# Optimization experiments

Measured on AMD Instinct MI355X. Metric: run time of the kernel, lower is better.

The kernel has to match this reference:

```python
import jax, jax.numpy as jnp
import numpy as np

N = 20000      # nodes
G = 400        # distinct TCR group ids
D_IN, H1, H2, D_OUT = 128, 256, 256, 128
LN_EPS = 1e-5


def _init_linear(key, fan_in, fan_out):
    s = 1.0 / np.sqrt(fan_in)
    return jax.random.uniform(key, (fan_in, fan_out), jnp.float32, -s, s)


def setup_inputs() -> dict:
    key = jax.random.key(0)
    ks = jax.random.split(key, 6)
    x = jax.random.normal(ks[0], (N, D_IN), jnp.float32)
    idx_TCR = jax.random.randint(ks[1], (N,), 0, G, dtype=jnp.int64)
    W1 = _init_linear(ks[2], D_IN, H1)
    W2 = _init_linear(ks[3], H1, H2)
    W3 = _init_linear(ks[4], H2, D_OUT)
    b1 = jnp.zeros((H1,), jnp.float32)
    b2 = jnp.zeros((H2,), jnp.float32)
    b3 = jnp.zeros((D_OUT,), jnp.float32)
    gamma = jnp.ones((D_OUT,), jnp.float32)
    beta = jnp.zeros((D_OUT,), jnp.float32)
    return {"x": x, "idx_TCR": idx_TCR, "W1": W1, "b1": b1,
            "W2": W2, "b2": b2, "W3": W3, "b3": b3,
            "gamma": gamma, "beta": beta}


def _build_edges(idx_TCR):
    # construct_graph: connect node pairs with equal idx, upper triangle only
    # (directed src<tgt edges, as in the torch code), then append self-loops
    # as PyG GCNConv.gcn_norm does.
    idx = np.asarray(idx_TCR).reshape(-1)
    n = idx.shape[0]
    eq = idx[:, None] == idx[None, :]
    src, tgt = np.nonzero(np.triu(eq, k=1))
    loop = np.arange(n)
    row = jnp.asarray(np.concatenate([src, loop]))  # message source
    col = jnp.asarray(np.concatenate([tgt, loop]))  # message target
    return row, col, n


def _gcn_norm(row, col, n, dtype):
    # degree from incoming edges (incl. self-loops), symmetric normalization
    deg = jax.ops.segment_sum(jnp.ones(row.shape[0], dtype), col, num_segments=n)
    dis = jnp.where(deg > 0, jax.lax.rsqrt(deg), jnp.zeros_like(deg))
    return dis[row] * dis[col]  # [E]


def _gcn_conv(x, W, b, row, col, norm, n):
    h = x @ W                                   # [N, out]
    msg = h[row] * norm[:, None]                # gather + scale, [E, out]
    out = jax.ops.segment_sum(msg, col, num_segments=n)  # scatter-add
    return out + b


def reference(x, idx_TCR, W1, b1, W2, b2, W3, b3, gamma, beta):
    row, col, n = _build_edges(idx_TCR)
    norm = _gcn_norm(row, col, n, x.dtype)
    h = jax.nn.relu(_gcn_conv(x, W1, b1, row, col, norm, n))
    h = jax.nn.relu(_gcn_conv(h, W2, b2, row, col, norm, n))
    h = jax.nn.relu(_gcn_conv(h, W3, b3, row, col, norm, n))
    # LayerNorm over last dim
    mu = h.mean(axis=-1, keepdims=True)
    var = ((h - mu) ** 2).mean(axis=-1, keepdims=True)
    return (h - mu) * jax.lax.rsqrt(var + LN_EPS) * gamma + beta
```

## Files before the change

### kernel.cpp

```cpp
#include <hip/hip_runtime.h>
#include <hip/hip_bf16.h>

#define NN 20000
#define NG 400
#define D_IN 128
#define H1 256
#define H2 256
#define D_OUT 128
#define WT_ELEMS (D_IN * H1 + H1 * H2 + H2 * D_OUT)
#define MCAP 1024
#define WSLOT 256

#define STY 72
#define ST1 136
#define ST2 264
#define ST3 264
#define SF  132
#define REGB 36864

typedef __attribute__((ext_vector_type(8))) short short8;
typedef __attribute__((ext_vector_type(4))) short short4v;
typedef __attribute__((ext_vector_type(4))) float floatx4;

__device__ __forceinline__ short f2b(float f) {
    __hip_bfloat16 h = __float2bfloat16(f);
    return *(short*)&h;
}


__global__ __launch_bounds__(256) void wt_all(
    const float* __restrict__ W1, const float* __restrict__ W2,
    const float* __restrict__ W3, __hip_bfloat16* __restrict__ Wt1,
    __hip_bfloat16* __restrict__ Wt2, __hip_bfloat16* __restrict__ Wt3)
{
    int o = blockIdx.x * 256 + threadIdx.x;
    if (o < D_IN * H1) {
        int n = o / D_IN, k = o - n * D_IN;
        Wt1[o] = __float2bfloat16(W1[(size_t)k * H1 + n]);
    } else if (o < D_IN * H1 + H1 * H2) {
        int p = o - D_IN * H1;
        int n = p / H1, k = p - n * H1;
        Wt2[p] = __float2bfloat16(W2[(size_t)k * H2 + n]);
    } else if (o < WT_ELEMS) {
        int p = o - D_IN * H1 - H1 * H2;
        int n = p / H2, k = p - n * H2;
        Wt3[p] = __float2bfloat16(W3[(size_t)k * D_OUT + n]);
    }
}


__global__ __launch_bounds__(512) void fused_gcn(
    const float* __restrict__ x, const int* __restrict__ idx,
    const __hip_bfloat16* __restrict__ Wt1_,
    const __hip_bfloat16* __restrict__ Wt2_,
    const __hip_bfloat16* __restrict__ Wt3_,
    const float* __restrict__ b1, const float* __restrict__ b2,
    const float* __restrict__ b3,
    const float* __restrict__ gamma, const float* __restrict__ beta,
    float* __restrict__ out)
{
    __shared__ __align__(16) char RA[REGB];
    __shared__ __align__(16) char RB[REGB];
    __shared__ int mlist[MCAP];
    __shared__ int wcnt[8];

    int tid = threadIdx.x;
    int w = tid >> 6;
    int lane = tid & 63;
    int quad = lane >> 4;
    int l15 = lane & 15;
    int g = blockIdx.x;

    int* WS = (int*)RA;
    {
        int slice = w * 625;
        int wcount = 0;
        unsigned long long lowm = (1ull << lane) - 1ull;
#pragma unroll
        for (int b2i = 0; b2i < 2; ++b2i) {
            int4 v[5];
#pragma unroll
            for (int r = 0; r < 5; ++r) {
                int q = (b2i * 5 + r) * 64 + lane;
                v[r] = (q < 625) ? *(const int4*)&idx[(slice + q) * 4]
                                 : make_int4(-1, -1, -1, -1);
            }
#pragma unroll
            for (int r = 0; r < 5; ++r) {
                bool f0 = (v[r].x == g), f1 = (v[r].y == g);
                bool f2 = (v[r].z == g), f3 = (v[r].w == g);
                unsigned long long m0 = __ballot(f0), m1 = __ballot(f1);
                unsigned long long m2 = __ballot(f2), m3 = __ballot(f3);
                int p = wcount + __popcll(m0 & lowm) + __popcll(m1 & lowm)
                               + __popcll(m2 & lowm) + __popcll(m3 & lowm);
                int j0 = (slice + (b2i * 5 + r) * 64 + lane) * 4;
                int e0 = (int)f0, e1 = (int)f1, e2 = (int)f2;
                if (f0 && p < WSLOT)                WS[w * WSLOT + p] = j0;
                if (f1 && p + e0 < WSLOT)           WS[w * WSLOT + p + e0] = j0 + 1;
                if (f2 && p + e0 + e1 < WSLOT)      WS[w * WSLOT + p + e0 + e1] = j0 + 2;
                if (f3 && p + e0 + e1 + e2 < WSLOT) WS[w * WSLOT + p + e0 + e1 + e2] = j0 + 3;
                wcount += __popcll(m0) + __popcll(m1) + __popcll(m2) + __popcll(m3);
            }
        }
        if (lane == 0) wcnt[w] = min(wcount, WSLOT);
    }
    __syncthreads();
    int cnt = 0;
    {
        int myprefix = 0;
#pragma unroll
        for (int ww = 0; ww < 8; ++ww) {
            int c = wcnt[ww];
            if (ww < w) myprefix += c;
            cnt += c;
        }
        cnt = min(cnt, MCAP);
        int myc = wcnt[w];
        for (int k = lane; k < myc; k += 64) {
            int dstp = myprefix + k;
            if (dstp < MCAP) mlist[dstp] = WS[w * WSLOT + k];
        }
    }
    if (cnt <= 0) return;

    float2 gmv = *(const float2*)&gamma[lane * 2];
    float2 btv = *(const float2*)&beta[lane * 2];
    float4 bb1[2], bb2[2], bb3;
#pragma unroll
    for (int i = 0; i < 2; ++i) {
        bb1[i] = *(const float4*)&b1[(2 * w + i) * 16 + quad * 4];
        bb2[i] = *(const float4*)&b2[(2 * w + i) * 16 + quad * 4];
    }
    bb3 = *(const float4*)&b3[w * 16 + quad * 4];

    __syncthreads();

    auto ltfrag = [&](int nt, int k2) -> short8 {
        int thr = nt * 16 + l15 - k2 * 32 - quad * 8;
        short8 f;
#pragma unroll
        for (int e = 0; e < 8; ++e)
            f[e] = (e <= thr) ? (short)0x3F80 : (short)0;
        return f;
    };

    float c1[2][4], c2[2][4], c3[4];
#pragma unroll
    for (int r = 0; r < 4; ++r) {
        c1[0][r] = 0.f; c1[1][r] = 0.f;
        c2[0][r] = 0.f; c2[1][r] = 0.f;
        c3[r] = 0.f;
    }

    const short* wt1p = (const short*)Wt1_;
    const short* wt2p = (const short*)Wt2_;
    const short* wt3p = (const short*)Wt3_;

    for (int base = 0; base < cnt; base += 64) {
        asm("" : "+s"(wt1p), "+s"(wt2p), "+s"(wt3p));
        int mt = min(64, cnt - base);
        int par = (base >> 6) & 1;
        char* Rc = par ? RB : RA;
        char* Rd = par ? RA : RB;
        short* T1 = (short*)Rc;
        short* T2 = (short*)Rc;
        short* T3 = (short*)Rc;
        float* F  = (float*)Rc;
        short* Yt = (short*)Rd;

        float djn[4];
#pragma unroll
        for (int nt = 0; nt < 4; ++nt)
            djn[nt] = rsqrtf((float)(base + nt * 16 + l15 + 1));

        {
            int row = (lane >> 3) + 8 * w;
            int mr = base + row;
            int nid = mlist[mr < cnt ? mr : cnt - 1];
            float sdr = rsqrtf((float)(mr + 1));
            const float* xp = x + (size_t)nid * D_IN + (lane & 7) * 4;
#pragma unroll
            for (int t = 0; t < 4; ++t) {
                float4 v = *(const float4*)(xp + t * 32);
                short4v o;
                o[0] = f2b(v.x * sdr); o[1] = f2b(v.y * sdr);
                o[2] = f2b(v.z * sdr); o[3] = f2b(v.w * sdr);
                *(short4v*)&T1[row * ST1 + (lane & 7) * 4 + t * 32] = o;
            }
        }
        __syncthreads();

        {
            floatx4 acc[4][2];
#pragma unroll
            for (int i = 0; i < 4; ++i) { acc[i][0] = (floatx4)0.0f; acc[i][1] = (floatx4)0.0f; }
#pragma unroll
            for (int kk = 0; kk < 4; ++kk) {
                short8 a4[4], bw[2];
#pragma unroll
                for (int i = 0; i < 4; ++i)
                    a4[i] = *(const short8*)&T1[(i * 16 + l15) * ST1 + kk * 32 + quad * 8];
#pragma unroll
                for (int nt = 0; nt < 2; ++nt)
                    bw[nt] = *(const short8*)&wt1p[((size_t)((w * 2 + nt) * 16 + l15)) * D_IN + kk * 32 + quad * 8];
#pragma unroll
                for (int i = 0; i < 4; ++i)
#pragma unroll
                    for (int nt = 0; nt < 2; ++nt)
                        acc[i][nt] = __builtin_amdgcn_mfma_f32_16x16x32_bf16(
                            a4[i], bw[nt], acc[i][nt], 0, 0, 0);
            }
#pragma unroll
            for (int i = 0; i < 4; ++i)
#pragma unroll
                for (int nt = 0; nt < 2; ++nt) {
                    short4v o4;
#pragma unroll
                    for (int r = 0; r < 4; ++r) o4[r] = f2b(acc[i][nt][r]);
                    *(short4v*)&Yt[((w * 2 + nt) * 16 + l15) * STY + i * 16 + quad * 4] = o4;
                }
        }
        __syncthreads();

        {
            floatx4 acc[2][4];
#pragma unroll
            for (int i = 0; i < 2; ++i)
#pragma unroll
                for (int nt = 0; nt < 4; ++nt) acc[i][nt] = (floatx4)0.0f;
#pragma unroll
            for (int k2 = 0; k2 < 2; ++k2) {
                short8 af[2];
#pragma unroll
                for (int i = 0; i < 2; ++i)
                    af[i] = *(const short8*)&Yt[((2 * w + i) * 16 + l15) * STY + k2 * 32 + quad * 8];
#pragma unroll
                for (int nt = 0; nt < 4; ++nt) {
                    short8 lt = ltfrag(nt, k2);
#pragma unroll
                    for (int i = 0; i < 2; ++i)
                        acc[i][nt] = __builtin_amdgcn_mfma_f32_16x16x32_bf16(
                            af[i], lt, acc[i][nt], 0, 0, 0);
                }
            }
#pragma unroll
            for (int i = 0; i < 2; ++i) {
                float nc[4] = {0.f, 0.f, 0.f, 0.f};
#pragma unroll
                for (int nt = 0; nt < 4; ++nt) {
                    float tmp[4];
#pragma unroll
                    for (int r = 0; r < 4; ++r) tmp[r] = acc[i][nt][r] + c1[i][r];
                    if (nt == 3) {
#pragma unroll
                        for (int r = 0; r < 4; ++r) nc[r] = tmp[r];
                    }
                    short4v o4;
                    o4[0] = f2b(fmaxf(tmp[0] * djn[nt] + bb1[i].x, 0.0f) * djn[nt]);
                    o4[1] = f2b(fmaxf(tmp[1] * djn[nt] + bb1[i].y, 0.0f) * djn[nt]);
                    o4[2] = f2b(fmaxf(tmp[2] * djn[nt] + bb1[i].z, 0.0f) * djn[nt]);
                    o4[3] = f2b(fmaxf(tmp[3] * djn[nt] + bb1[i].w, 0.0f) * djn[nt]);
                    *(short4v*)&T2[(nt * 16 + l15) * ST2 + (2 * w + i) * 16 + quad * 4] = o4;
                }
#pragma unroll
                for (int r = 0; r < 4; ++r)
                    c1[i][r] = __shfl(nc[r], (lane & 48) + 15);
            }
        }
        __syncthreads();

        {
            floatx4 acc[4][2];
#pragma unroll
            for (int i = 0; i < 4; ++i) { acc[i][0] = (floatx4)0.0f; acc[i][1] = (floatx4)0.0f; }
#pragma unroll
            for (int kk = 0; kk < 8; ++kk) {
                short8 a4[4], bw[2];
#pragma unroll
                for (int i = 0; i < 4; ++i)
                    a4[i] = *(const short8*)&T2[(i * 16 + l15) * ST2 + kk * 32 + quad * 8];
#pragma unroll
                for (int nt = 0; nt < 2; ++nt)
                    bw[nt] = *(const short8*)&wt2p[((size_t)((w * 2 + nt) * 16 + l15)) * H1 + kk * 32 + quad * 8];
#pragma unroll
                for (int i = 0; i < 4; ++i)
#pragma unroll
                    for (int nt = 0; nt < 2; ++nt)
                        acc[i][nt] = __builtin_amdgcn_mfma_f32_16x16x32_bf16(
                            a4[i], bw[nt], acc[i][nt], 0, 0, 0);
            }
#pragma unroll
            for (int i = 0; i < 4; ++i)
#pragma unroll
                for (int nt = 0; nt < 2; ++nt) {
                    short4v o4;
#pragma unroll
                    for (int r = 0; r < 4; ++r) o4[r] = f2b(acc[i][nt][r]);
                    *(short4v*)&Yt[((w * 2 + nt) * 16 + l15) * STY + i * 16 + quad * 4] = o4;
                }
        }
        __syncthreads();

        {
            floatx4 acc[2][4];
#pragma unroll
            for (int i = 0; i < 2; ++i)
#pragma unroll
                for (int nt = 0; nt < 4; ++nt) acc[i][nt] = (floatx4)0.0f;
#pragma unroll
            for (int k2 = 0; k2 < 2; ++k2) {
                short8 af[2];
#pragma unroll
                for (int i = 0; i < 2; ++i)
                    af[i] = *(const short8*)&Yt[((2 * w + i) * 16 + l15) * STY + k2 * 32 + quad * 8];
#pragma unroll
                for (int nt = 0; nt < 4; ++nt) {
                    short8 lt = ltfrag(nt, k2);
#pragma unroll
                    for (int i = 0; i < 2; ++i)
                        acc[i][nt] = __builtin_amdgcn_mfma_f32_16x16x32_bf16(
                            af[i], lt, acc[i][nt], 0, 0, 0);
                }
            }
#pragma unroll
            for (int i = 0; i < 2; ++i) {
                float nc[4] = {0.f, 0.f, 0.f, 0.f};
#pragma unroll
                for (int nt = 0; nt < 4; ++nt) {
                    float tmp[4];
#pragma unroll
                    for (int r = 0; r < 4; ++r) tmp[r] = acc[i][nt][r] + c2[i][r];
                    if (nt == 3) {
#pragma unroll
                        for (int r = 0; r < 4; ++r) nc[r] = tmp[r];
                    }
                    short4v o4;
                    o4[0] = f2b(fmaxf(tmp[0] * djn[nt] + bb2[i].x, 0.0f) * djn[nt]);
                    o4[1] = f2b(fmaxf(tmp[1] * djn[nt] + bb2[i].y, 0.0f) * djn[nt]);
                    o4[2] = f2b(fmaxf(tmp[2] * djn[nt] + bb2[i].z, 0.0f) * djn[nt]);
                    o4[3] = f2b(fmaxf(tmp[3] * djn[nt] + bb2[i].w, 0.0f) * djn[nt]);
                    *(short4v*)&T3[(nt * 16 + l15) * ST3 + (2 * w + i) * 16 + quad * 4] = o4;
                }
#pragma unroll
                for (int r = 0; r < 4; ++r)
                    c2[i][r] = __shfl(nc[r], (lane & 48) + 15);
            }
        }
        __syncthreads();

        {
            floatx4 acc[4];
#pragma unroll
            for (int i = 0; i < 4; ++i) acc[i] = (floatx4)0.0f;
#pragma unroll
            for (int kk = 0; kk < 8; ++kk) {
                short8 bw = *(const short8*)&wt3p[((size_t)(w * 16 + l15)) * H2 + kk * 32 + quad * 8];
#pragma unroll
                for (int i = 0; i < 4; ++i) {
                    short8 a4 = *(const short8*)&T3[(i * 16 + l15) * ST3 + kk * 32 + quad * 8];
                    acc[i] = __builtin_amdgcn_mfma_f32_16x16x32_bf16(a4, bw, acc[i], 0, 0, 0);
                }
            }
#pragma unroll
            for (int i = 0; i < 4; ++i) {
                short4v o4;
#pragma unroll
                for (int r = 0; r < 4; ++r) o4[r] = f2b(acc[i][r]);
                *(short4v*)&Yt[(w * 16 + l15) * STY + i * 16 + quad * 4] = o4;
            }
        }
        __syncthreads();

        {
            floatx4 acc[4];
#pragma unroll
            for (int nt = 0; nt < 4; ++nt) acc[nt] = (floatx4)0.0f;
#pragma unroll
            for (int k2 = 0; k2 < 2; ++k2) {
                short8 af = *(const short8*)&Yt[(w * 16 + l15) * STY + k2 * 32 + quad * 8];
#pragma unroll
                for (int nt = 0; nt < 4; ++nt)
                    acc[nt] = __builtin_amdgcn_mfma_f32_16x16x32_bf16(
                        af, ltfrag(nt, k2), acc[nt], 0, 0, 0);
            }
            float nc[4] = {0.f, 0.f, 0.f, 0.f};
#pragma unroll
            for (int nt = 0; nt < 4; ++nt) {
                float tmp[4];
#pragma unroll
                for (int r = 0; r < 4; ++r) tmp[r] = acc[nt][r] + c3[r];
                if (nt == 3) {
#pragma unroll
                    for (int r = 0; r < 4; ++r) nc[r] = tmp[r];
                }
                float4 o;
                o.x = fmaxf(tmp[0] * djn[nt] + bb3.x, 0.0f);
                o.y = fmaxf(tmp[1] * djn[nt] + bb3.y, 0.0f);
                o.z = fmaxf(tmp[2] * djn[nt] + bb3.z, 0.0f);
                o.w = fmaxf(tmp[3] * djn[nt] + bb3.w, 0.0f);
                *(float4*)&F[(nt * 16 + l15) * SF + w * 16 + quad * 4] = o;
            }
#pragma unroll
            for (int r = 0; r < 4; ++r)
                c3[r] = __shfl(nc[r], (lane & 48) + 15);
        }
        __syncthreads();

        for (int r = w; r < mt; r += 8) {
            float2 v = *(const float2*)&F[r * SF + lane * 2];
            float s1 = v.x + v.y;
            float s2v = v.x * v.x + v.y * v.y;
#pragma unroll
            for (int off = 32; off > 0; off >>= 1) {
                s1 += __shfl_down(s1, off);
                s2v += __shfl_down(s2v, off);
            }
            s1 = __shfl(s1, 0);
            s2v = __shfl(s2v, 0);
            float mu = s1 * (1.0f / D_OUT);
            float var = s2v * (1.0f / D_OUT) - mu * mu;
            float rstd = rsqrtf(var + 1e-5f);
            float2 o;
            o.x = (v.x - mu) * rstd * gmv.x + btv.x;
            o.y = (v.y - mu) * rstd * gmv.y + btv.y;
            *(float2*)&out[(size_t)mlist[base + r] * D_OUT + lane * 2] = o;
        }
    }
}


extern "C" void kernel_launch(void* const* d_in, const int* in_sizes, int n_in,
                              void* d_out, int out_size, void* d_ws, size_t ws_size,
                              hipStream_t stream) {
    const float* x     = (const float*)d_in[0];
    const int*   idx   = (const int*)d_in[1];
    const float* W1    = (const float*)d_in[2];
    const float* b1    = (const float*)d_in[3];
    const float* W2    = (const float*)d_in[4];
    const float* b2    = (const float*)d_in[5];
    const float* W3    = (const float*)d_in[6];
    const float* b3    = (const float*)d_in[7];
    const float* gamma = (const float*)d_in[8];
    const float* beta  = (const float*)d_in[9];
    float* out = (float*)d_out;

    char* ws = (char*)d_ws;
    size_t off = 0;
    auto alloc = [&](size_t bytes) -> void* {
        void* p = (void*)(ws + off);
        off += (bytes + 255) & ~(size_t)255;
        return p;
    };
    __hip_bfloat16* Wt1 = (__hip_bfloat16*)alloc((size_t)D_IN * H1 * 2);
    __hip_bfloat16* Wt2 = (__hip_bfloat16*)alloc((size_t)H1 * H2 * 2);
    __hip_bfloat16* Wt3 = (__hip_bfloat16*)alloc((size_t)H2 * D_OUT * 2);

    wt_all<<<(WT_ELEMS + 255) / 256, 256, 0, stream>>>(
        W1, W2, W3, Wt1, Wt2, Wt3);

    fused_gcn<<<NG, 512, 0, stream>>>(
        x, idx, Wt1, Wt2, Wt3, b1, b2, b3, gamma, beta, out);
}
```

Baseline: 127.5 us.

## Process two groups per block with four waves each

Each block now handles two TCR groups, with the 8 waves split into two teams of 4, each team doing twice the column work per stage. The grid is halved to 200 blocks, which fits a single wave of blocks on the CUs and halves the per-block idx scan cost per group. LDS doubles to about 147KB, so occupancy stays at one block per CU. Each team does twice the serial MFMA work, and the loop runs to the larger of the two group counts, so the block waits on its slower group.

```diff
diff --git a/kernel.cpp b/kernel.cpp
--- a/kernel.cpp
+++ b/kernel.cpp
@@ -8,7 +8,7 @@
 #define H2 256
 #define D_OUT 128
 #define WT_ELEMS (D_IN * H1 + H1 * H2 + H2 * D_OUT)
-#define MCAP 1024
+#define MC2 512
 #define WSLOT 256
 
 #define STY 72
@@ -16,7 +16,7 @@
 #define ST2 264
 #define ST3 264
 #define SF  132
-#define REGB 36864
+#define PIPEB 73728
 
 typedef __attribute__((ext_vector_type(8))) short short8;
 typedef __attribute__((ext_vector_type(4))) short short4v;
@@ -59,22 +59,25 @@
     const float* __restrict__ gamma, const float* __restrict__ beta,
     float* __restrict__ out)
 {
-    __shared__ __align__(16) char RA[REGB];
-    __shared__ __align__(16) char RB[REGB];
-    __shared__ int mlist[MCAP];
-    __shared__ int wcnt[8];
+    __shared__ __align__(16) char LB[2 * PIPEB];
+    __shared__ int mlist0[MC2], mlist1[MC2];
+    __shared__ int wcnt0[8], wcnt1[8];
 
     int tid = threadIdx.x;
     int w = tid >> 6;
     int lane = tid & 63;
     int quad = lane >> 4;
     int l15 = lane & 15;
-    int g = blockIdx.x;
-
-    int* WS = (int*)RA;
+    int p = w >> 2;
+    int u = w & 3;
+    int g0 = blockIdx.x * 2;
+    int g1 = g0 + 1;
+
+    int* WS0 = (int*)LB;
+    int* WS1 = (int*)(LB + 8192);
     {
         int slice = w * 625;
-        int wcount = 0;
+        int wc0 = 0, wc1 = 0;
         unsigned long long lowm = (1ull << lane) - 1ull;
 #pragma unroll
         for (int b2i = 0; b2i < 2; ++b2i) {
@@ -87,53 +90,71 @@
             }
 #pragma unroll
             for (int r = 0; r < 5; ++r) {
-                bool f0 = (v[r].x == g), f1 = (v[r].y == g);
-                bool f2 = (v[r].z == g), f3 = (v[r].w == g);
-                unsigned long long m0 = __ballot(f0), m1 = __ballot(f1);
-                unsigned long long m2 = __ballot(f2), m3 = __ballot(f3);
-                int p = wcount + __popcll(m0 & lowm) + __popcll(m1 & lowm)
-                               + __popcll(m2 & lowm) + __popcll(m3 & lowm);
                 int j0 = (slice + (b2i * 5 + r) * 64 + lane) * 4;
-                int e0 = (int)f0, e1 = (int)f1, e2 = (int)f2;
-                if (f0 && p < WSLOT)                WS[w * WSLOT + p] = j0;
-                if (f1 && p + e0 < WSLOT)           WS[w * WSLOT + p + e0] = j0 + 1;
-                if (f2 && p + e0 + e1 < WSLOT)      WS[w * WSLOT + p + e0 + e1] = j0 + 2;
-                if (f3 && p + e0 + e1 + e2 < WSLOT) WS[w * WSLOT + p + e0 + e1 + e2] = j0 + 3;
-                wcount += __popcll(m0) + __popcll(m1) + __popcll(m2) + __popcll(m3);
-            }
-        }
-        if (lane == 0) wcnt[w] = min(wcount, WSLOT);
+                {
+                    bool f0 = (v[r].x == g0), f1 = (v[r].y == g0);
+                    bool f2 = (v[r].z == g0), f3 = (v[r].w == g0);
+                    unsigned long long m0 = __ballot(f0), m1 = __ballot(f1);
+                    unsigned long long m2 = __ballot(f2), m3 = __ballot(f3);
+                    int pp = wc0 + __popcll(m0 & lowm) + __popcll(m1 & lowm)
+                                 + __popcll(m2 & lowm) + __popcll(m3 & lowm);
+                    int e0 = (int)f0, e1 = (int)f1, e2 = (int)f2;
+                    if (f0 && pp < WSLOT)                WS0[w * WSLOT + pp] = j0;
+                    if (f1 && pp + e0 < WSLOT)           WS0[w * WSLOT + pp + e0] = j0 + 1;
+                    if (f2 && pp + e0 + e1 < WSLOT)      WS0[w * WSLOT + pp + e0 + e1] = j0 + 2;
+                    if (f3 && pp + e0 + e1 + e2 < WSLOT) WS0[w * WSLOT + pp + e0 + e1 + e2] = j0 + 3;
+                    wc0 += __popcll(m0) + __popcll(m1) + __popcll(m2) + __popcll(m3);
+                }
+                {
+                    bool f0 = (v[r].x == g1), f1 = (v[r].y == g1);
+                    bool f2 = (v[r].z == g1), f3 = (v[r].w == g1);
+                    unsigned long long m0 = __ballot(f0), m1 = __ballot(f1);
+                    unsigned long long m2 = __ballot(f2), m3 = __ballot(f3);
+                    int pp = wc1 + __popcll(m0 & lowm) + __popcll(m1 & lowm)
+                                 + __popcll(m2 & lowm) + __popcll(m3 & lowm);
+                    int e0 = (int)f0, e1 = (int)f1, e2 = (int)f2;
+                    if (f0 && pp < WSLOT)                WS1[w * WSLOT + pp] = j0;
+                    if (f1 && pp + e0 < WSLOT)           WS1[w * WSLOT + pp + e0] = j0 + 1;
+                    if (f2 && pp + e0 + e1 < WSLOT)      WS1[w * WSLOT + pp + e0 + e1] = j0 + 2;
+                    if (f3 && pp + e0 + e1 + e2 < WSLOT) WS1[w * WSLOT + pp + e0 + e1 + e2] = j0 + 3;
+                    wc1 += __popcll(m0) + __popcll(m1) + __popcll(m2) + __popcll(m3);
+                }
+            }
+        }
+        if (lane == 0) { wcnt0[w] = min(wc0, WSLOT); wcnt1[w] = min(wc1, WSLOT); }
     }
     __syncthreads();
-    int cnt = 0;
+    int cnt0 = 0, cnt1 = 0;
     {
-        int myprefix = 0;
+        int pre0 = 0, pre1 = 0;
 #pragma unroll
         for (int ww = 0; ww < 8; ++ww) {
-            int c = wcnt[ww];
-            if (ww < w) myprefix += c;
-            cnt += c;
-        }
-        cnt = min(cnt, MCAP);
-        int myc = wcnt[w];
-        for (int k = lane; k < myc; k += 64) {
-            int dstp = myprefix + k;
-            if (dstp < MCAP) mlist[dstp] = WS[w * WSLOT + k];
+            int c0 = wcnt0[ww], c1w = wcnt1[ww];
+            if (ww < w) { pre0 += c0; pre1 += c1w; }
+            cnt0 += c0; cnt1 += c1w;
+        }
+        cnt0 = min(cnt0, MC2); cnt1 = min(cnt1, MC2);
+        int myc0 = wcnt0[w], myc1 = wcnt1[w];
+        for (int k = lane; k < myc0; k += 64) {
+            int dstp = pre0 + k;
+            if (dstp < MC2) mlist0[dstp] = WS0[w * WSLOT + k];
+        }
+        for (int k = lane; k < myc1; k += 64) {
+            int dstp = pre1 + k;
+            if (dstp < MC2) mlist1[dstp] = WS1[w * WSLOT + k];
         }
     }
-    if (cnt <= 0) return;
+    int cmax = max(cnt0, cnt1);
+    if (cmax <= 0) return;
 
     float2 gmv = *(const float2*)&gamma[lane * 2];
     float2 btv = *(const float2*)&beta[lane * 2];
-    float4 bb1[2], bb2[2], bb3;
-#pragma unroll
-    for (int i = 0; i < 2; ++i) {
-        bb1[i] = *(const float4*)&b1[(2 * w + i) * 16 + quad * 4];
-        bb2[i] = *(const float4*)&b2[(2 * w + i) * 16 + quad * 4];
-    }
-    bb3 = *(const float4*)&b3[w * 16 + quad * 4];
 
     __syncthreads();
+
+    int mycnt = p ? cnt1 : cnt0;
+    int* mylist = p ? mlist1 : mlist0;
+    char* PB = LB + p * PIPEB;
 
     auto ltfrag = [&](int nt, int k2) -> short8 {
         int thr = nt * 16 + l15 - k2 * 32 - quad * 8;
@@ -144,24 +165,26 @@
         return f;
     };
 
-    float c1[2][4], c2[2][4], c3[4];
-#pragma unroll
-    for (int r = 0; r < 4; ++r) {
-        c1[0][r] = 0.f; c1[1][r] = 0.f;
-        c2[0][r] = 0.f; c2[1][r] = 0.f;
-        c3[r] = 0.f;
-    }
+    float c1[2][2][4], c2[2][2][4], c3[2][4];
+#pragma unroll
+    for (int hf = 0; hf < 2; ++hf)
+#pragma unroll
+        for (int r = 0; r < 4; ++r) {
+            c1[hf][0][r] = 0.f; c1[hf][1][r] = 0.f;
+            c2[hf][0][r] = 0.f; c2[hf][1][r] = 0.f;
+            c3[hf][r] = 0.f;
+        }
 
     const short* wt1p = (const short*)Wt1_;
     const short* wt2p = (const short*)Wt2_;
     const short* wt3p = (const short*)Wt3_;
 
-    for (int base = 0; base < cnt; base += 64) {
+    for (int base = 0; base < cmax; base += 64) {
         asm("" : "+s"(wt1p), "+s"(wt2p), "+s"(wt3p));
-        int mt = min(64, cnt - base);
+        int mt = min(64, mycnt - base);
         int par = (base >> 6) & 1;
-        char* Rc = par ? RB : RA;
-        char* Rd = par ? RA : RB;
+        char* Rc = PB + (par ? 36864 : 0);
+        char* Rd = PB + (par ? 0 : 36864);
         short* T1 = (short*)Rc;
         short* T2 = (short*)Rc;
         short* T3 = (short*)Rc;
@@ -173,10 +196,13 @@
         for (int nt = 0; nt < 4; ++nt)
             djn[nt] = rsqrtf((float)(base + nt * 16 + l15 + 1));
 
-        {
-            int row = (lane >> 3) + 8 * w;
+#pragma unroll
+        for (int hf = 0; hf < 2; ++hf) {
+            int hw = hf * 4 + u;
+            int row = (lane >> 3) + 8 * hw;
             int mr = base + row;
-            int nid = mlist[mr < cnt ? mr : cnt - 1];
+            int mi = (mr < mycnt) ? mr : (mycnt > 0 ? mycnt - 1 : 0);
+            int nid = (mycnt > 0) ? mylist[mi] : 0;
             float sdr = rsqrtf((float)(mr + 1));
             const float* xp = x + (size_t)nid * D_IN + (lane & 7) * 4;
 #pragma unroll
@@ -190,7 +216,9 @@
         }
         __syncthreads();
 
-        {
+#pragma unroll
+        for (int hf = 0; hf < 2; ++hf) {
+            int hw = hf * 4 + u;
             floatx4 acc[4][2];
 #pragma unroll
             for (int i = 0; i < 4; ++i) { acc[i][0] = (floatx4)0.0f; acc[i][1] = (floatx4)0.0f; }
@@ -202,7 +230,7 @@
                     a4[i] = *(const short8*)&T1[(i * 16 + l15) * ST1 + kk * 32 + quad * 8];
 #pragma unroll
                 for (int nt = 0; nt < 2; ++nt)
-                    bw[nt] = *(const short8*)&wt1p[((size_t)((w * 2 + nt) * 16 + l15)) * D_IN + kk * 32 + quad * 8];
+                    bw[nt] = *(const short8*)&wt1p[((size_t)((hw * 2 + nt) * 16 + l15)) * D_IN + kk * 32 + quad * 8];
 #pragma unroll
                 for (int i = 0; i < 4; ++i)
 #pragma unroll
@@ -217,12 +245,14 @@
                     short4v o4;
 #pragma unroll
                     for (int r = 0; r < 4; ++r) o4[r] = f2b(acc[i][nt][r]);
-                    *(short4v*)&Yt[((w * 2 + nt) * 16 + l15) * STY + i * 16 + quad * 4] = o4;
-                }
-        }
-        __syncthreads();
-
-        {
+                    *(short4v*)&Yt[((hw * 2 + nt) * 16 + l15) * STY + i * 16 + quad * 4] = o4;
+                }
+        }
+        __syncthreads();
+
+#pragma unroll
+        for (int hf = 0; hf < 2; ++hf) {
+            int hw = hf * 4 + u;
             floatx4 acc[2][4];
 #pragma unroll
             for (int i = 0; i < 2; ++i)
@@ -233,7 +263,7 @@
                 short8 af[2];
 #pragma unroll
                 for (int i = 0; i < 2; ++i)
-                    af[i] = *(const short8*)&Yt[((2 * w + i) * 16 + l15) * STY + k2 * 32 + quad * 8];
+                    af[i] = *(const short8*)&Yt[((2 * hw + i) * 16 + l15) * STY + k2 * 32 + quad * 8];
 #pragma unroll
                 for (int nt = 0; nt < 4; ++nt) {
                     short8 lt = ltfrag(nt, k2);
@@ -245,31 +275,34 @@
             }
 #pragma unroll
             for (int i = 0; i < 2; ++i) {
+                float4 bb = *(const float4*)&b1[(2 * hw + i) * 16 + quad * 4];
                 float nc[4] = {0.f, 0.f, 0.f, 0.f};
 #pragma unroll
                 for (int nt = 0; nt < 4; ++nt) {
                     float tmp[4];
 #pragma unroll
-                    for (int r = 0; r < 4; ++r) tmp[r] = acc[i][nt][r] + c1[i][r];
+                    for (int r = 0; r < 4; ++r) tmp[r] = acc[i][nt][r] + c1[hf][i][r];
                     if (nt == 3) {
 #pragma unroll
                         for (int r = 0; r < 4; ++r) nc[r] = tmp[r];
                     }
                     short4v o4;
-                    o4[0] = f2b(fmaxf(tmp[0] * djn[nt] + bb1[i].x, 0.0f) * djn[nt]);
-                    o4[1] = f2b(fmaxf(tmp[1] * djn[nt] + bb1[i].y, 0.0f) * djn[nt]);
-                    o4[2] = f2b(fmaxf(tmp[2] * djn[nt] + bb1[i].z, 0.0f) * djn[nt]);
-                    o4[3] = f2b(fmaxf(tmp[3] * djn[nt] + bb1[i].w, 0.0f) * djn[nt]);
-                    *(short4v*)&T2[(nt * 16 + l15) * ST2 + (2 * w + i) * 16 + quad * 4] = o4;
+                    o4[0] = f2b(fmaxf(tmp[0] * djn[nt] + bb.x, 0.0f) * djn[nt]);
+                    o4[1] = f2b(fmaxf(tmp[1] * djn[nt] + bb.y, 0.0f) * djn[nt]);
+                    o4[2] = f2b(fmaxf(tmp[2] * djn[nt] + bb.z, 0.0f) * djn[nt]);
+                    o4[3] = f2b(fmaxf(tmp[3] * djn[nt] + bb.w, 0.0f) * djn[nt]);
+                    *(short4v*)&T2[(nt * 16 + l15) * ST2 + (2 * hw + i) * 16 + quad * 4] = o4;
                 }
 #pragma unroll
                 for (int r = 0; r < 4; ++r)
-                    c1[i][r] = __shfl(nc[r], (lane & 48) + 15);
-            }
-        }
-        __syncthreads();
-
-        {
+                    c1[hf][i][r] = __shfl(nc[r], (lane & 48) + 15);
+            }
+        }
+        __syncthreads();
+
+#pragma unroll
+        for (int hf = 0; hf < 2; ++hf) {
+            int hw = hf * 4 + u;
             floatx4 acc[4][2];
 #pragma unroll
             for (int i = 0; i < 4; ++i) { acc[i][0] = (floatx4)0.0f; acc[i][1] = (floatx4)0.0f; }
@@ -281,7 +314,7 @@
                     a4[i] = *(const short8*)&T2[(i * 16 + l15) * ST2 + kk * 32 + quad * 8];
 #pragma unroll
                 for (int nt = 0; nt < 2; ++nt)
-                    bw[nt] = *(const short8*)&wt2p[((size_t)((w * 2 + nt) * 16 + l15)) * H1 + kk * 32 + quad * 8];
+                    bw[nt] = *(const short8*)&wt2p[((size_t)((hw * 2 + nt) * 16 + l15)) * H1 + kk * 32 + quad * 8];
 #pragma unroll
                 for (int i = 0; i < 4; ++i)
 #pragma unroll
@@ -296,12 +329,14 @@
                     short4v o4;
 #pragma unroll
                     for (int r = 0; r < 4; ++r) o4[r] = f2b(acc[i][nt][r]);
-                    *(short4v*)&Yt[((w * 2 + nt) * 16 + l15) * STY + i * 16 + quad * 4] = o4;
-                }
-        }
-        __syncthreads();
-
-        {
+                    *(short4v*)&Yt[((hw * 2 + nt) * 16 + l15) * STY + i * 16 + quad * 4] = o4;
+                }
+        }
+        __syncthreads();
+
+#pragma unroll
+        for (int hf = 0; hf < 2; ++hf) {
+            int hw = hf * 4 + u;
             floatx4 acc[2][4];
 #pragma unroll
             for (int i = 0; i < 2; ++i)
@@ -312,7 +347,7 @@
                 short8 af[2];
 #pragma unroll
                 for (int i = 0; i < 2; ++i)
-                    af[i] = *(const short8*)&Yt[((2 * w + i) * 16 + l15) * STY + k2 * 32 + quad * 8];
+                    af[i] = *(const short8*)&Yt[((2 * hw + i) * 16 + l15) * STY + k2 * 32 + quad * 8];
 #pragma unroll
                 for (int nt = 0; nt < 4; ++nt) {
                     short8 lt = ltfrag(nt, k2);
@@ -324,37 +359,40 @@
             }
 #pragma unroll
             for (int i = 0; i < 2; ++i) {
+                float4 bb = *(const float4*)&b2[(2 * hw + i) * 16 + quad * 4];
                 float nc[4] = {0.f, 0.f, 0.f, 0.f};
 #pragma unroll
                 for (int nt = 0; nt < 4; ++nt) {
                     float tmp[4];
 #pragma unroll
-                    for (int r = 0; r < 4; ++r) tmp[r] = acc[i][nt][r] + c2[i][r];
+                    for (int r = 0; r < 4; ++r) tmp[r] = acc[i][nt][r] + c2[hf][i][r];
                     if (nt == 3) {
 #pragma unroll
                         for (int r = 0; r < 4; ++r) nc[r] = tmp[r];
                     }
                     short4v o4;
-                    o4[0] = f2b(fmaxf(tmp[0] * djn[nt] + bb2[i].x, 0.0f) * djn[nt]);
-                    o4[1] = f2b(fmaxf(tmp[1] * djn[nt] + bb2[i].y, 0.0f) * djn[nt]);
-                    o4[2] = f2b(fmaxf(tmp[2] * djn[nt] + bb2[i].z, 0.0f) * djn[nt]);
-                    o4[3] = f2b(fmaxf(tmp[3] * djn[nt] + bb2[i].w, 0.0f) * djn[nt]);
-                    *(short4v*)&T3[(nt * 16 + l15) * ST3 + (2 * w + i) * 16 + quad * 4] = o4;
+                    o4[0] = f2b(fmaxf(tmp[0] * djn[nt] + bb.x, 0.0f) * djn[nt]);
+                    o4[1] = f2b(fmaxf(tmp[1] * djn[nt] + bb.y, 0.0f) * djn[nt]);
+                    o4[2] = f2b(fmaxf(tmp[2] * djn[nt] + bb.z, 0.0f) * djn[nt]);
+                    o4[3] = f2b(fmaxf(tmp[3] * djn[nt] + bb.w, 0.0f) * djn[nt]);
+                    *(short4v*)&T3[(nt * 16 + l15) * ST3 + (2 * hw + i) * 16 + quad * 4] = o4;
                 }
 #pragma unroll
                 for (int r = 0; r < 4; ++r)
-                    c2[i][r] = __shfl(nc[r], (lane & 48) + 15);
-            }
-        }
-        __syncthreads();
-
-        {
+                    c2[hf][i][r] = __shfl(nc[r], (lane & 48) + 15);
+            }
+        }
+        __syncthreads();
+
+#pragma unroll
+        for (int hf = 0; hf < 2; ++hf) {
+            int hw = hf * 4 + u;
             floatx4 acc[4];
 #pragma unroll
             for (int i = 0; i < 4; ++i) acc[i] = (floatx4)0.0f;
 #pragma unroll
             for (int kk = 0; kk < 8; ++kk) {
-                short8 bw = *(const short8*)&wt3p[((size_t)(w * 16 + l15)) * H2 + kk * 32 + quad * 8];
+                short8 bw = *(const short8*)&wt3p[((size_t)(hw * 16 + l15)) * H2 + kk * 32 + quad * 8];
 #pragma unroll
                 for (int i = 0; i < 4; ++i) {
                     short8 a4 = *(const short8*)&T3[(i * 16 + l15) * ST3 + kk * 32 + quad * 8];
@@ -366,64 +404,71 @@
                 short4v o4;
 #pragma unroll
                 for (int r = 0; r < 4; ++r) o4[r] = f2b(acc[i][r]);
-                *(short4v*)&Yt[(w * 16 + l15) * STY + i * 16 + quad * 4] = o4;
-            }
-        }
-        __syncthreads();
-
-        {
+                *(short4v*)&Yt[(hw * 16 + l15) * STY + i * 16 + quad * 4] = o4;
+            }
+        }
+        __syncthreads();
+
+#pragma unroll
+        for (int hf = 0; hf < 2; ++hf) {
+            int hw = hf * 4 + u;
             floatx4 acc[4];
 #pragma unroll
             for (int nt = 0; nt < 4; ++nt) acc[nt] = (floatx4)0.0f;
 #pragma unroll
             for (int k2 = 0; k2 < 2; ++k2) {
-                short8 af = *(const short8*)&Yt[(w * 16 + l15) * STY + k2 * 32 + quad * 8];
+                short8 af = *(const short8*)&Yt[(hw * 16 + l15) * STY + k2 * 32 + quad * 8];
 #pragma unroll
                 for (int nt = 0; nt < 4; ++nt)
                     acc[nt] = __builtin_amdgcn_mfma_f32_16x16x32_bf16(
                         af, ltfrag(nt, k2), acc[nt], 0, 0, 0);
             }
+            float4 bb = *(const float4*)&b3[hw * 16 + quad * 4];
             float nc[4] = {0.f, 0.f, 0.f, 0.f};
 #pragma unroll
             for (int nt = 0; nt < 4; ++nt) {
                 float tmp[4];
 #pragma unroll
-                for (int r = 0; r < 4; ++r) tmp[r] = acc[nt][r] + c3[r];
+                for (int r = 0; r < 4; ++r) tmp[r] = acc[nt][r] + c3[hf][r];
                 if (nt == 3) {
 #pragma unroll
                     for (int r = 0; r < 4; ++r) nc[r] = tmp[r];
                 }
                 float4 o;
-                o.x = fmaxf(tmp[0] * djn[nt] + bb3.x, 0.0f);
-                o.y = fmaxf(tmp[1] * djn[nt] + bb3.y, 0.0f);
-                o.z = fmaxf(tmp[2] * djn[nt] + bb3.z, 0.0f);
-                o.w = fmaxf(tmp[3] * djn[nt] + bb3.w, 0.0f);
-                *(float4*)&F[(nt * 16 + l15) * SF + w * 16 + quad * 4] = o;
+                o.x = fmaxf(tmp[0] * djn[nt] + bb.x, 0.0f);
+                o.y = fmaxf(tmp[1] * djn[nt] + bb.y, 0.0f);
+                o.z = fmaxf(tmp[2] * djn[nt] + bb.z, 0.0f);
+                o.w = fmaxf(tmp[3] * djn[nt] + bb.w, 0.0f);
+                *(float4*)&F[(nt * 16 + l15) * SF + hw * 16 + quad * 4] = o;
             }
 #pragma unroll
             for (int r = 0; r < 4; ++r)
-                c3[r] = __shfl(nc[r], (lane & 48) + 15);
-        }
-        __syncthreads();
-
-        for (int r = w; r < mt; r += 8) {
-            float2 v = *(const float2*)&F[r * SF + lane * 2];
-            float s1 = v.x + v.y;
-            float s2v = v.x * v.x + v.y * v.y;
-#pragma unroll
-            for (int off = 32; off > 0; off >>= 1) {
-                s1 += __shfl_down(s1, off);
-                s2v += __shfl_down(s2v, off);
-            }
-            s1 = __shfl(s1, 0);
-            s2v = __shfl(s2v, 0);
-            float mu = s1 * (1.0f / D_OUT);
-            float var = s2v * (1.0f / D_OUT) - mu * mu;
-            float rstd = rsqrtf(var + 1e-5f);
-            float2 o;
-            o.x = (v.x - mu) * rstd * gmv.x + btv.x;
-            o.y = (v.y - mu) * rstd * gmv.y + btv.y;
-            *(float2*)&out[(size_t)mlist[base + r] * D_OUT + lane * 2] = o;
+                c3[hf][r] = __shfl(nc[r], (lane & 48) + 15);
+        }
+        __syncthreads();
+
+#pragma unroll
+        for (int hf = 0; hf < 2; ++hf) {
+            int hw = hf * 4 + u;
+            for (int r = hw; r < mt; r += 8) {
+                float2 v = *(const float2*)&F[r * SF + lane * 2];
+                float s1 = v.x + v.y;
+                float s2v = v.x * v.x + v.y * v.y;
+#pragma unroll
+                for (int off = 32; off > 0; off >>= 1) {
+                    s1 += __shfl_down(s1, off);
+                    s2v += __shfl_down(s2v, off);
+                }
+                s1 = __shfl(s1, 0);
+                s2v = __shfl(s2v, 0);
+                float mu = s1 * (1.0f / D_OUT);
+                float var = s2v * (1.0f / D_OUT) - mu * mu;
+                float rstd = rsqrtf(var + 1e-5f);
+                float2 o;
+                o.x = (v.x - mu) * rstd * gmv.x + btv.x;
+                o.y = (v.y - mu) * rstd * gmv.y + btv.y;
+                *(float2*)&out[(size_t)mylist[base + r] * D_OUT + lane * 2] = o;
+            }
         }
     }
 }
@@ -458,6 +503,6 @@
     wt_all<<<(WT_ELEMS + 255) / 256, 256, 0, stream>>>(
         W1, W2, W3, Wt1, Wt2, Wt3);
 
-    fused_gcn<<<NG, 512, 0, stream>>>(
+    fused_gcn<<<NG / 2, 512, 0, stream>>>(
         x, idx, Wt1, Wt2, Wt3, b1, b2, b3, gamma, beta, out);
 }
```

Measured after the change: 134.9 us. +5.8%, slower.
